# Kernel tuning notes

Hardware: AMD Instinct MI355X
Metric: run time of the kernel (lower is better)

The kernel has to match this reference:

```python
import jax, jax.numpy as jnp
import numpy as np

B, D, N = 512, 512, 196  # batch, hidden dim, kb elements (14x14 feature grid)


def setup_inputs() -> dict:
    key = jax.random.key(0)
    ks = jax.random.split(key, 8)
    s = 1.0 / np.sqrt(D)
    return {
        "memory_state": jax.random.normal(ks[0], (B, D), jnp.float32),
        "knowledge_base": jax.random.normal(ks[1], (B, D, N), jnp.float32),
        "ctrl_state": jax.random.normal(ks[2], (B, D), jnp.float32),
        "kb_proj": jax.random.normal(ks[3], (B, D, N), jnp.float32),
        "W_mem": jax.random.normal(ks[4], (D, D), jnp.float32) * s,
        "b_mem": jnp.zeros((D,), jnp.float32),
        "W_cat": jax.random.normal(ks[5], (D, 2 * D), jnp.float32) * s,
        "b_cat": jnp.zeros((D,), jnp.float32),
        "W_attn": jax.random.normal(ks[6], (1, D), jnp.float32) * s,
        "b_attn": jnp.zeros((1,), jnp.float32),
    }


def reference(memory_state, knowledge_base, ctrl_state, kb_proj,
              W_mem, b_mem, W_cat, b_cat, W_attn, b_attn):
    # mem projection: [B, D]
    mem = memory_state @ W_mem.T + b_mem
    # interaction with projected knowledge base: [B, D, N]
    I_elements = mem[:, :, None] * kb_proj
    # concat along channel dim -> [B, 2D, N], permute to [B, N, 2D]
    cat = jnp.concatenate([I_elements, knowledge_base], axis=1).transpose(0, 2, 1)
    # concat layer: [B, N, D]
    concat = cat @ W_cat.T + b_cat
    # gate by control state, attention logits: [B, N]
    rai = ((concat * ctrl_state[:, None, :]) @ W_attn.T + b_attn)[:, :, 0]
    rvi = jax.nn.softmax(rai, axis=1)  # [B, N]
    # weighted sum over kb elements: [B, D]
    read_vector = jnp.einsum('bn,bdn->bd', rvi, knowledge_base)
    return read_vector
```

## Files before the change

### kernel.cpp

```cpp
#include <hip/hip_runtime.h>
#include <hip/hip_bf16.h>


constexpr int D = 512;
constexpr int N = 196;

__global__ __launch_bounds__(256) void phase_a(
    const float* __restrict__ ms, const float* __restrict__ ctrl,
    const float* __restrict__ Wmem, const float* __restrict__ bmem,
    const float* __restrict__ Wcat, const float* __restrict__ Wattn,
    float* __restrict__ mem_ws, float* __restrict__ v_ws)
{
    constexpr int PAD = 68;
    __shared__ float As[16 * PAD];
    __shared__ float Bs[16 * PAD];

    const int bid = blockIdx.x;
    const int t   = threadIdx.x;
    const int tx  = t & 15, ty = t >> 4;

    const bool g1 = (bid < 64);
    int tile_m, tile_n;
    if (g1) { tile_m = (bid >> 3) * 64; tile_n = (bid & 7) * 64; }
    else    { int bb = bid - 64; tile_m = (bb >> 4) * 64; tile_n = (bb & 15) * 64; }

    float acc[4][4] = {};

    for (int k0 = 0; k0 < 512; k0 += 16) {
        {
            const int k = t & 15;
            const int mbase = t >> 4;
#pragma unroll
            for (int r = 0; r < 4; r++) {
                const int m = mbase + 16 * r;
                const int row = tile_m + m;
                float a;
                if (g1) a = ms[row * 512 + k0 + k];
                else    a = ctrl[row * 512 + k0 + k] * Wattn[k0 + k];
                As[k * PAD + m] = a;
            }
        }
        if (g1) {
            const int k = t & 15;
            const int nbase = t >> 4;
#pragma unroll
            for (int r = 0; r < 4; r++) {
                const int n = nbase + 16 * r;
                Bs[k * PAD + n] = Wmem[(tile_n + n) * 512 + k0 + k];
            }
        } else {
            const int n = t & 63;
            const int kbase = t >> 6;
#pragma unroll
            for (int r = 0; r < 4; r++) {
                const int k = kbase + 4 * r;
                Bs[k * PAD + n] = Wcat[(k0 + k) * 1024 + tile_n + n];
            }
        }
        __syncthreads();
#pragma unroll
        for (int k = 0; k < 16; k++) {
            const float4 av = *reinterpret_cast<const float4*>(&As[k * PAD + ty * 4]);
            const float4 bv = *reinterpret_cast<const float4*>(&Bs[k * PAD + tx * 4]);
            const float a[4] = {av.x, av.y, av.z, av.w};
            const float bb[4] = {bv.x, bv.y, bv.z, bv.w};
#pragma unroll
            for (int i = 0; i < 4; i++)
#pragma unroll
                for (int j = 0; j < 4; j++)
                    acc[i][j] += a[i] * bb[j];
        }
        __syncthreads();
    }

    if (g1) {
#pragma unroll
        for (int i = 0; i < 4; i++) {
            const int row = tile_m + ty * 4 + i;
#pragma unroll
            for (int j = 0; j < 4; j++) {
                const int col = tile_n + tx * 4 + j;
                mem_ws[row * 512 + col] = acc[i][j] + bmem[col];
            }
        }
    } else {
#pragma unroll
        for (int i = 0; i < 4; i++) {
            const int row = tile_m + ty * 4 + i;
#pragma unroll
            for (int j = 0; j < 4; j++) {
                const int col = tile_n + tx * 4 + j;
                v_ws[row * 1024 + col] = acc[i][j];
            }
        }
    }
}

__global__ __launch_bounds__(256, 2) void phase_b(
    const float* __restrict__ kb,
    const float* __restrict__ kbp,
    const float* __restrict__ mem_ws,
    const float* __restrict__ v_ws,
    float* __restrict__ out)
{
    constexpr int C = 14;
    constexpr int P = 516;
    __shared__ float kbs[C * P];
    __shared__ float kps[C * P];
    __shared__ float rai_s[C];

    const int b    = blockIdx.x;
    const int t    = threadIdx.x;
    const int lane = t & 63;
    const int wave = t >> 6;

    const float* kb_b  = kb  + (size_t)b * D * N;
    const float* kbp_b = kbp + (size_t)b * D * N;

    float p_r[8], q_r[8];
#pragma unroll
    for (int k = 0; k < 8; k++) {
        const int d = lane + 64 * k;
        const float m  = mem_ws[b * D + d];
        const float v1 = v_ws[b * 2 * D + d];
        p_r[k] = m * v1;
        q_r[k] = v_ws[b * 2 * D + D + d];
    }

    float acc0 = 0.f, acc1 = 0.f, L = 0.f;

    for (int c = 0; c < 14; c++) {
        const int n0 = c * C;
#pragma unroll
        for (int i = 0; i < 28; i++) {
            const int idx = i * 256 + t;
            const int d = idx / 14;
            const int n = idx - d * 14;
            const size_t g = (size_t)d * N + n0 + n;
            kps[n * P + d] = kbp_b[g];
            kbs[n * P + d] = kb_b[g];
        }
        __syncthreads();

#pragma unroll
        for (int j = 0; j < 4; j++) {
            const int n = wave * 4 + j;
            if (n < C) {
                float s = 0.f;
#pragma unroll
                for (int k = 0; k < 8; k++) {
                    const int d = lane + 64 * k;
                    s += p_r[k] * kps[n * P + d] + q_r[k] * kbs[n * P + d];
                }
#pragma unroll
                for (int m = 32; m; m >>= 1) s += __shfl_xor(s, m, 64);
                if (lane == 0) rai_s[n] = s;
            }
        }
        __syncthreads();

        float w[C];
        float wsum = 0.f;
#pragma unroll
        for (int n = 0; n < C; n++) { w[n] = __expf(rai_s[n]); wsum += w[n]; }
        L += wsum;
#pragma unroll
        for (int n = 0; n < C; n++) {
            acc0 += w[n] * kbs[n * P + t];
            acc1 += w[n] * kbs[n * P + t + 256];
        }
        __syncthreads();
    }

    const float inv = 1.0f / L;
    out[b * D + t]       = acc0 * inv;
    out[b * D + t + 256] = acc1 * inv;
}

extern "C" void kernel_launch(void* const* d_in, const int* in_sizes, int n_in,
                              void* d_out, int out_size, void* d_ws, size_t ws_size,
                              hipStream_t stream) {
    const float* ms    = (const float*)d_in[0];
    const float* kb    = (const float*)d_in[1];
    const float* ctrl  = (const float*)d_in[2];
    const float* kbp   = (const float*)d_in[3];
    const float* Wmem  = (const float*)d_in[4];
    const float* bmem  = (const float*)d_in[5];
    const float* Wcat  = (const float*)d_in[6];
    const float* Wattn = (const float*)d_in[8];

    float* mem_ws = (float*)d_ws;
    float* v_ws   = mem_ws + 512 * 512;

    phase_a<<<192, 256, 0, stream>>>(ms, ctrl, Wmem, bmem, Wcat, Wattn, mem_ws, v_ws);
    phase_b<<<512, 256, 0, stream>>>(kb, kbp, mem_ws, v_ws, (float*)d_out);
}
```

Measured before the change: 553.5 us.

## Split attention into vectorized logit and weighted-sum kernels with float4 streaming

Replaces the single per-batch kernel, which staged kb and kb_proj chunks through shared memory, with two kernels. The first computes the attention logits by streaming both tensors with coalesced float4 loads, splitting D across two blocks per batch. The second applies the softmax and the weighted sum, re-reading kb in reverse batch order to favour cache reuse. This trades an extra pass over kb for much better memory coalescing and parallelism.

```diff
diff --git a/kernel.cpp b/kernel.cpp
--- a/kernel.cpp
+++ b/kernel.cpp
@@ -4,6 +4,9 @@
 
 constexpr int D = 512;
 constexpr int N = 196;
+constexpr int NF4 = 49;
+
+using f4 = __attribute__((ext_vector_type(4))) float;
 
 __global__ __launch_bounds__(256) void phase_a(
     const float* __restrict__ ms, const float* __restrict__ ctrl,
@@ -96,85 +99,115 @@
     }
 }
 
-__global__ __launch_bounds__(256, 2) void phase_b(
-    const float* __restrict__ kb,
-    const float* __restrict__ kbp,
-    const float* __restrict__ mem_ws,
-    const float* __restrict__ v_ws,
+__global__ __launch_bounds__(256) void k_rai(
+    const f4* __restrict__ kb, const f4* __restrict__ kbp,
+    const float* __restrict__ mem_ws, const float* __restrict__ v_ws,
+    float* __restrict__ rai_ws)
+{
+    __shared__ float p_s[256];
+    __shared__ float q_s[256];
+    __shared__ float part[4][200];
+
+    const int bid = blockIdx.x;
+    const int b   = bid >> 1;
+    const int s   = bid & 1;
+    const int d0  = s * 256;
+    const int t    = threadIdx.x;
+    const int lane = t & 63;
+    const int w    = t >> 6;
+
+    {
+        const int d = d0 + t;
+        p_s[t] = mem_ws[b * D + d] * v_ws[b * 2 * D + d];
+        q_s[t] = v_ws[b * 2 * D + D + d];
+    }
+    __syncthreads();
+
+    const int lc = (lane < NF4) ? lane : (NF4 - 1);
+    const f4* kb_b  = kb  + (size_t)b * (D * NF4);
+    const f4* kbp_b = kbp + (size_t)b * (D * NF4);
+
+    float a0 = 0.f, a1 = 0.f, a2 = 0.f, a3 = 0.f;
+    const int dw = d0 + w * 64;
+#pragma unroll 4
+    for (int r = 0; r < 64; r++) {
+        const int d = dw + r;
+        const f4 vp = __builtin_nontemporal_load(&kbp_b[(size_t)d * NF4 + lc]);
+        const f4 vk = kb_b[(size_t)d * NF4 + lc];
+        const float pd = p_s[d - d0];
+        const float qd = q_s[d - d0];
+        a0 += pd * vp.x + qd * vk.x;
+        a1 += pd * vp.y + qd * vk.y;
+        a2 += pd * vp.z + qd * vk.z;
+        a3 += pd * vp.w + qd * vk.w;
+    }
+
+    if (lane < NF4) {
+        part[w][4 * lane + 0] = a0;
+        part[w][4 * lane + 1] = a1;
+        part[w][4 * lane + 2] = a2;
+        part[w][4 * lane + 3] = a3;
+    }
+    __syncthreads();
+
+    if (t < N) {
+        const float r = part[0][t] + part[1][t] + part[2][t] + part[3][t];
+        rai_ws[(size_t)(b * 2 + s) * N + t] = r;
+    }
+}
+
+__global__ __launch_bounds__(256) void k_out(
+    const f4* __restrict__ kb, const float* __restrict__ rai_ws,
     float* __restrict__ out)
 {
-    constexpr int C = 14;
-    constexpr int P = 516;
-    __shared__ float kbs[C * P];
-    __shared__ float kps[C * P];
-    __shared__ float rai_s[C];
-
-    const int b    = blockIdx.x;
+    __shared__ float w_s[N];
+    __shared__ float red[4];
+    __shared__ float out_s[D];
+
+    const int b    = 511 - (int)blockIdx.x;
     const int t    = threadIdx.x;
     const int lane = t & 63;
-    const int wave = t >> 6;
-
-    const float* kb_b  = kb  + (size_t)b * D * N;
-    const float* kbp_b = kbp + (size_t)b * D * N;
-
-    float p_r[8], q_r[8];
-#pragma unroll
-    for (int k = 0; k < 8; k++) {
-        const int d = lane + 64 * k;
-        const float m  = mem_ws[b * D + d];
-        const float v1 = v_ws[b * 2 * D + d];
-        p_r[k] = m * v1;
-        q_r[k] = v_ws[b * 2 * D + D + d];
-    }
-
-    float acc0 = 0.f, acc1 = 0.f, L = 0.f;
-
-    for (int c = 0; c < 14; c++) {
-        const int n0 = c * C;
-#pragma unroll
-        for (int i = 0; i < 28; i++) {
-            const int idx = i * 256 + t;
-            const int d = idx / 14;
-            const int n = idx - d * 14;
-            const size_t g = (size_t)d * N + n0 + n;
-            kps[n * P + d] = kbp_b[g];
-            kbs[n * P + d] = kb_b[g];
-        }
-        __syncthreads();
-
-#pragma unroll
-        for (int j = 0; j < 4; j++) {
-            const int n = wave * 4 + j;
-            if (n < C) {
-                float s = 0.f;
-#pragma unroll
-                for (int k = 0; k < 8; k++) {
-                    const int d = lane + 64 * k;
-                    s += p_r[k] * kps[n * P + d] + q_r[k] * kbs[n * P + d];
-                }
-#pragma unroll
-                for (int m = 32; m; m >>= 1) s += __shfl_xor(s, m, 64);
-                if (lane == 0) rai_s[n] = s;
-            }
-        }
-        __syncthreads();
-
-        float w[C];
-        float wsum = 0.f;
-#pragma unroll
-        for (int n = 0; n < C; n++) { w[n] = __expf(rai_s[n]); wsum += w[n]; }
-        L += wsum;
-#pragma unroll
-        for (int n = 0; n < C; n++) {
-            acc0 += w[n] * kbs[n * P + t];
-            acc1 += w[n] * kbs[n * P + t + 256];
-        }
-        __syncthreads();
-    }
-
-    const float inv = 1.0f / L;
-    out[b * D + t]       = acc0 * inv;
-    out[b * D + t + 256] = acc1 * inv;
+    const int w    = t >> 6;
+
+    float e = 0.f;
+    if (t < N) {
+        const float r = rai_ws[(size_t)(b * 2) * N + t]
+                      + rai_ws[(size_t)(b * 2 + 1) * N + t];
+        e = __expf(r);
+        w_s[t] = e;
+    }
+    float ssum = e;
+#pragma unroll
+    for (int m = 32; m; m >>= 1) ssum += __shfl_xor(ssum, m, 64);
+    if (lane == 0) red[w] = ssum;
+    __syncthreads();
+
+    const float inv = 1.0f / (red[0] + red[1] + red[2] + red[3]);
+
+    f4 wv = {0.f, 0.f, 0.f, 0.f};
+    if (lane < NF4) {
+        wv.x = w_s[4 * lane + 0] * inv;
+        wv.y = w_s[4 * lane + 1] * inv;
+        wv.z = w_s[4 * lane + 2] * inv;
+        wv.w = w_s[4 * lane + 3] * inv;
+    }
+
+    const int lc = (lane < NF4) ? lane : (NF4 - 1);
+    const f4* kb_b = kb + (size_t)b * (D * NF4);
+    const int dw = w * 128;
+#pragma unroll 4
+    for (int r = 0; r < 128; r++) {
+        const int d = dw + r;
+        const f4 v = kb_b[(size_t)d * NF4 + lc];
+        float sc = v.x * wv.x + v.y * wv.y + v.z * wv.z + v.w * wv.w;
+#pragma unroll
+        for (int m = 32; m; m >>= 1) sc += __shfl_xor(sc, m, 64);
+        if (lane == 0) out_s[d] = sc;
+    }
+    __syncthreads();
+
+    out[(size_t)b * D + t]       = out_s[t];
+    out[(size_t)b * D + 256 + t] = out_s[256 + t];
 }
 
 extern "C" void kernel_launch(void* const* d_in, const int* in_sizes, int n_in,
@@ -191,7 +224,9 @@
 
     float* mem_ws = (float*)d_ws;
     float* v_ws   = mem_ws + 512 * 512;
+    float* rai_ws = v_ws + 512 * 1024;
 
     phase_a<<<192, 256, 0, stream>>>(ms, ctrl, Wmem, bmem, Wcat, Wattn, mem_ws, v_ws);
-    phase_b<<<512, 256, 0, stream>>>(kb, kbp, mem_ws, v_ws, (float*)d_out);
-}
+    k_rai<<<1024, 256, 0, stream>>>((const f4*)kb, (const f4*)kbp, mem_ws, v_ws, rai_ws);
+    k_out<<<512, 256, 0, stream>>>((const f4*)kb, rai_ws, (float*)d_out);
+}
```

Result: no change. 545.7 us (-1.4%).
